# Kernel tuning notes

Hardware: AMD Instinct MI355X
Metric: run time of the kernel (lower is better)

Reference implementation:

```python
import jax, jax.numpy as jnp
import numpy as np

N = 8192
D = 128
NUM_CLASSES = 16
EPS = 1e-8  # torch cosine_similarity eps


def setup_inputs() -> dict:
    key = jax.random.key(0)
    k1, k2 = jax.random.split(key)
    inp = jax.random.normal(k1, (N, D), dtype=jnp.float32)
    targets = jax.random.randint(k2, (N,), 0, NUM_CLASSES, dtype=jnp.int64)
    temperature = jnp.asarray(0.5, dtype=jnp.float32)
    return {"input": inp, "targets": targets, "temperature": temperature}


def reference(input, targets, temperature):
    # clamp temperature to [0.1, 1.0] as the module does in forward
    temp = jnp.clip(temperature, 0.1, 1.0)

    # cosine similarity matrix [N, N]
    norms = jnp.maximum(jnp.linalg.norm(input, axis=1, keepdims=True), EPS)
    xn = input / norms
    sim = jnp.matmul(xn, xn.T) / temp          # [N, N]
    E = jnp.exp(sim)                            # [N, N]

    same = targets[:, None] == targets[None, :]  # [N, N] bool
    diag = jnp.diagonal(E)                       # exp(s_ii)
    pos = jnp.sum(jnp.where(same, E, 0.0), axis=1) - diag   # same-class, excl self
    tot = jnp.sum(E, axis=1) - diag                          # pos + neg
    per_sample_loss = -jnp.log(pos / tot)                    # [N]

    # per-class aggregation (segment sums with static num_segments)
    counts = jax.ops.segment_sum(jnp.ones_like(per_sample_loss), targets,
                                 num_segments=NUM_CLASSES)
    sums = jax.ops.segment_sum(per_sample_loss, targets,
                               num_segments=NUM_CLASSES)
    safe_counts = jnp.maximum(counts, 1.0)
    class_mean = sums / safe_counts

    # class weights: (1/count) normalized over present classes
    inv = jnp.where(counts > 0, 1.0 / safe_counts, 0.0)
    weights = inv / jnp.sum(inv)

    # only classes with more than one sample contribute
    valid = counts > 1
    weighted = jnp.where(valid, class_mean * weights, 0.0)
    n_valid = jnp.sum(valid.astype(jnp.float32))
    loss = jnp.sum(weighted) / n_valid
    return loss
```

## Files before the change

kernel.cpp:

```cpp
#include <hip/hip_runtime.h>

#define N 8192
#define D 128
#define NCLS 16
#define SLOT 512
#define RSTRIDE 256

typedef unsigned short u16;
typedef __attribute__((ext_vector_type(8))) short v8s;
typedef __attribute__((ext_vector_type(16))) float f32x16;

static __device__ inline u16 f2bf(float f) {
  unsigned int u = __builtin_bit_cast(unsigned int, f);
  unsigned int r = u + 0x7fffu + ((u >> 16) & 1u);
  return (u16)(r >> 16);
}

__global__ __launch_bounds__(256) void k_norm(float* __restrict__ buf,
                                              const float* __restrict__ temp) {
  int wave = threadIdx.x >> 6;
  int lane = threadIdx.x & 63;
  int row = blockIdx.x * 4 + wave;
  const float* p = buf + (size_t)row * D + lane * 2;
  float x = p[0], y = p[1];
  float ss = x * x + y * y;
#pragma unroll
  for (int m = 32; m >= 1; m >>= 1) ss += __shfl_xor(ss, m);
  float t = fminf(fmaxf(temp[0], 0.1f), 1.0f);
  float sc = sqrtf(1.4426950408889634f / t);
  float inv = sc / fmaxf(sqrtf(ss), 1e-8f);
  unsigned int u0 = (unsigned int)f2bf(x * inv);
  unsigned int u1 = (unsigned int)f2bf(y * inv);
  reinterpret_cast<unsigned int*>(buf)[(size_t)row * 128 + lane] = u0 | (u1 << 16);
}

__global__ __launch_bounds__(256, 3) void k_sim(float* __restrict__ buf,
                                                const int* __restrict__ tgt) {
  __shared__ __align__(16) char lds[2][64 * 256];
  __shared__ float red_pos[4][32];
  __shared__ float red_tot[4][32];

  const int tid = threadIdx.x;
  const int wave = tid >> 6;
  const int lane = tid & 63;
  const int l31 = lane & 31;
  const int h = lane >> 5;

  const u16* xnb = reinterpret_cast<const u16*>(buf);

  const int rowstrip = blockIdx.x >> 3;
  const int cq = blockIdx.x & 7;
  const int rwb = rowstrip * 64 + (wave >> 1) * 32;
  const int colblock = cq * 1024;
  const int ch = wave & 1;

  v8s afrag[8];
  {
    const u16* ap = xnb + (size_t)(rwb + l31) * RSTRIDE + h * 8;
#pragma unroll
    for (int kk = 0; kk < 8; ++kk)
      afrag[kk] = *reinterpret_cast<const v8s*>(ap + kk * 16);
  }

  int trow[16];
#pragma unroll
  for (int r = 0; r < 16; ++r)
    trow[r] = tgt[rwb + ((r & 3) + 8 * (r >> 2) + 4 * h)];

  float tot_acc[16], pos_acc[16];
#pragma unroll
  for (int r = 0; r < 16; ++r) { tot_acc[r] = 0.f; pos_acc[r] = 0.f; }

  auto stage = [&](int g, int bsel) {
    int rowbase = colblock + g * 64;
#pragma unroll
    for (int i = 0; i < 4; ++i) {
      int L = i * 256 + tid;
      int row = L >> 4;
      int s = (L & 15) ^ (row & 15);
      const char* src = reinterpret_cast<const char*>(buf) +
                        (size_t)(rowbase + row) * SLOT + s * 16;
      char* dst = &lds[bsel][(i * 256 + wave * 64) * 16];
      __builtin_amdgcn_global_load_lds(
          (const __attribute__((address_space(1))) void*)src,
          (__attribute__((address_space(3))) void*)dst, 16, 0, 0);
    }
  };

  stage(0, 0);
  __syncthreads();

  const int lr = ch * 32 + l31;
  const int lbase = lr * 256;
  const int lm = lr & 15;

  for (int g = 0; g < 16; ++g) {
    int cur = g & 1;
    if (g + 1 < 16) stage(g + 1, cur ^ 1);

    int c0 = colblock + g * 64 + ch * 32;
    int tcol = tgt[c0 + l31];

    f32x16 acc;
#pragma unroll
    for (int r = 0; r < 16; ++r) acc[r] = 0.f;
    const char* lb = lds[cur];
#pragma unroll
    for (int kk = 0; kk < 8; ++kk) {
      v8s bf = *reinterpret_cast<const v8s*>(lb + lbase + (((2 * kk + h) ^ lm) << 4));
      acc = __builtin_amdgcn_mfma_f32_32x32x16_bf16(afrag[kk], bf, acc, 0, 0, 0);
    }

    if (c0 != rwb) {
#pragma unroll
      for (int r = 0; r < 16; ++r) {
        float e = exp2f(acc[r]);
        tot_acc[r] += e;
        pos_acc[r] += (tcol == trow[r]) ? e : 0.f;
      }
    } else {
#pragma unroll
      for (int r = 0; r < 16; ++r) {
        float e = exp2f(acc[r]);
        if (l31 == ((r & 3) + 8 * (r >> 2) + 4 * h)) e = 0.f;
        tot_acc[r] += e;
        pos_acc[r] += (tcol == trow[r]) ? e : 0.f;
      }
    }
    __syncthreads();
  }

#pragma unroll
  for (int r = 0; r < 16; ++r) {
    float p = pos_acc[r], q = tot_acc[r];
#pragma unroll
    for (int m = 1; m <= 16; m <<= 1) {
      p += __shfl_xor(p, m);
      q += __shfl_xor(q, m);
    }
    if (l31 == 0) {
      int rl = (r & 3) + 8 * (r >> 2) + 4 * h;
      red_pos[wave][rl] = p;
      red_tot[wave][rl] = q;
    }
  }
  __syncthreads();
  if (tid < 64) {
    int gg = tid >> 5, rl = tid & 31;
    int row = rowstrip * 64 + gg * 32 + rl;
    float p = red_pos[2 * gg][rl] + red_pos[2 * gg + 1][rl];
    float q = red_tot[2 * gg][rl] + red_tot[2 * gg + 1][rl];
    float* slot = reinterpret_cast<float*>(reinterpret_cast<char*>(buf) + (size_t)row * SLOT + 256);
    slot[cq] = p;
    slot[8 + cq] = q;
  }
}

__global__ __launch_bounds__(1024) void k_tail(const float* __restrict__ buf,
                                               const int* __restrict__ tgt,
                                               float* __restrict__ out) {
  __shared__ float cs[NCLS], cc[NCLS];
  int tid = threadIdx.x;
  if (tid < NCLS) { cs[tid] = 0.f; cc[tid] = 0.f; }
  __syncthreads();
#pragma unroll
  for (int j = 0; j < 8; ++j) {
    int row = j * 1024 + tid;
    const float4* s4 = reinterpret_cast<const float4*>(
        reinterpret_cast<const char*>(buf) + (size_t)row * SLOT + 256);
    float4 a = s4[0], b = s4[1], c4 = s4[2], d4 = s4[3];
    float pos = a.x + a.y + a.z + a.w + b.x + b.y + b.z + b.w;
    float tot = c4.x + c4.y + c4.z + c4.w + d4.x + d4.y + d4.z + d4.w;
    float loss = logf(tot) - logf(pos);
    int c = tgt[row];
    atomicAdd(&cs[c], loss);
    atomicAdd(&cc[c], 1.0f);
  }
  __syncthreads();
  if (tid < 64) {
    int c = tid;
    float s = 0.f, n = 0.f;
    if (c < NCLS) { s = cs[c]; n = cc[c]; }
    float safe = fmaxf(n, 1.0f);
    float mean = s / safe;
    float inv = (n > 0.5f) ? 1.0f / safe : 0.f;
    float valid = (n > 1.5f) ? 1.f : 0.f;
    float w = (n > 1.5f) ? mean * inv : 0.f;
    float sinv = inv, sw = w, sv = valid;
#pragma unroll
    for (int m = 1; m <= 32; m <<= 1) {
      sinv += __shfl_xor(sinv, m);
      sw += __shfl_xor(sw, m);
      sv += __shfl_xor(sv, m);
    }
    if (c == 0) out[0] = sw / sinv / sv;
  }
}

extern "C" void kernel_launch(void* const* d_in, const int* in_sizes, int n_in,
                              void* d_out, int out_size, void* d_ws, size_t ws_size,
                              hipStream_t stream) {
  float* buf = (float*)d_in[0];
  const int* tgt = (const int*)d_in[1];
  const float* temp = (const float*)d_in[2];
  float* out = (float*)d_out;
  (void)d_ws; (void)ws_size;

  k_norm<<<N / 4, 256, 0, stream>>>(buf, temp);
  k_sim<<<1024, 256, 0, stream>>>(buf, tgt);
  k_tail<<<1, 1024, 0, stream>>>(buf, tgt, out);
}
```

Measured before the change: 131.3 us.

## Retile similarity kernel to 128x256 blocks and split tail reduction across blocks

Each k_sim block now covers 128 rows by 256 columns. All four waves share one 32-column B tile staged into LDS per step, where before each tile was shared by two waves. Each wave writes its row partials straight to global, which removes the shared-memory cross-wave reduction and one barrier, and the grid doubles to 2048 blocks. The single-block tail is replaced by 64 blocks that compute per-class partial sums, followed by a tiny final kernel. The trade-offs are more partial slots per row (32 instead of 8), more global writes, and one extra kernel launch.

New measurement: 112.6 us. -14.3%, faster.

```diff
diff --git a/kernel.cpp b/kernel.cpp
--- a/kernel.cpp
+++ b/kernel.cpp
@@ -34,25 +34,23 @@
   reinterpret_cast<unsigned int*>(buf)[(size_t)row * 128 + lane] = u0 | (u1 << 16);
 }
 
-__global__ __launch_bounds__(256, 3) void k_sim(float* __restrict__ buf,
-                                                const int* __restrict__ tgt) {
-  __shared__ __align__(16) char lds[2][64 * 256];
-  __shared__ float red_pos[4][32];
-  __shared__ float red_tot[4][32];
+__global__ __launch_bounds__(256) void k_sim(float* __restrict__ buf,
+                                             const int* __restrict__ tgt) {
+  __shared__ __align__(16) char lds[2][32 * 256];
 
   const int tid = threadIdx.x;
   const int wave = tid >> 6;
   const int lane = tid & 63;
   const int l31 = lane & 31;
   const int h = lane >> 5;
+  const int lm = l31 & 15;
 
   const u16* xnb = reinterpret_cast<const u16*>(buf);
 
-  const int rowstrip = blockIdx.x >> 3;
-  const int cq = blockIdx.x & 7;
-  const int rwb = rowstrip * 64 + (wave >> 1) * 32;
-  const int colblock = cq * 1024;
-  const int ch = wave & 1;
+  const int rowstrip = blockIdx.x >> 5;
+  const int cq = blockIdx.x & 31;
+  const int rwb = rowstrip * 128 + wave * 32;
+  const int colblock = cq * 256;
 
   v8s afrag[8];
   {
@@ -72,9 +70,9 @@
   for (int r = 0; r < 16; ++r) { tot_acc[r] = 0.f; pos_acc[r] = 0.f; }
 
   auto stage = [&](int g, int bsel) {
-    int rowbase = colblock + g * 64;
-#pragma unroll
-    for (int i = 0; i < 4; ++i) {
+    int rowbase = colblock + g * 32;
+#pragma unroll
+    for (int i = 0; i < 2; ++i) {
       int L = i * 256 + tid;
       int row = L >> 4;
       int s = (L & 15) ^ (row & 15);
@@ -90,15 +88,13 @@
   stage(0, 0);
   __syncthreads();
 
-  const int lr = ch * 32 + l31;
-  const int lbase = lr * 256;
-  const int lm = lr & 15;
-
-  for (int g = 0; g < 16; ++g) {
+  const int lbase = l31 * 256;
+
+  for (int g = 0; g < 8; ++g) {
     int cur = g & 1;
-    if (g + 1 < 16) stage(g + 1, cur ^ 1);
-
-    int c0 = colblock + g * 64 + ch * 32;
+    if (g + 1 < 8) stage(g + 1, cur ^ 1);
+
+    int c0 = colblock + g * 32;
     int tcol = tgt[c0 + l31];
 
     f32x16 acc;
@@ -139,42 +135,55 @@
       q += __shfl_xor(q, m);
     }
     if (l31 == 0) {
-      int rl = (r & 3) + 8 * (r >> 2) + 4 * h;
-      red_pos[wave][rl] = p;
-      red_tot[wave][rl] = q;
-    }
-  }
-  __syncthreads();
-  if (tid < 64) {
-    int gg = tid >> 5, rl = tid & 31;
-    int row = rowstrip * 64 + gg * 32 + rl;
-    float p = red_pos[2 * gg][rl] + red_pos[2 * gg + 1][rl];
-    float q = red_tot[2 * gg][rl] + red_tot[2 * gg + 1][rl];
-    float* slot = reinterpret_cast<float*>(reinterpret_cast<char*>(buf) + (size_t)row * SLOT + 256);
-    slot[cq] = p;
-    slot[8 + cq] = q;
-  }
-}
-
-__global__ __launch_bounds__(1024) void k_tail(const float* __restrict__ buf,
-                                               const int* __restrict__ tgt,
-                                               float* __restrict__ out) {
+      int row = rwb + ((r & 3) + 8 * (r >> 2) + 4 * h);
+      float* slot = reinterpret_cast<float*>(
+          reinterpret_cast<char*>(buf) + (size_t)row * SLOT + 256);
+      slot[cq] = p;
+      slot[32 + cq] = q;
+    }
+  }
+}
+
+__global__ __launch_bounds__(128) void k_tail_a(float* __restrict__ buf,
+                                                const int* __restrict__ tgt) {
   __shared__ float cs[NCLS], cc[NCLS];
   int tid = threadIdx.x;
   if (tid < NCLS) { cs[tid] = 0.f; cc[tid] = 0.f; }
   __syncthreads();
-#pragma unroll
-  for (int j = 0; j < 8; ++j) {
-    int row = j * 1024 + tid;
-    const float4* s4 = reinterpret_cast<const float4*>(
-        reinterpret_cast<const char*>(buf) + (size_t)row * SLOT + 256);
-    float4 a = s4[0], b = s4[1], c4 = s4[2], d4 = s4[3];
-    float pos = a.x + a.y + a.z + a.w + b.x + b.y + b.z + b.w;
-    float tot = c4.x + c4.y + c4.z + c4.w + d4.x + d4.y + d4.z + d4.w;
-    float loss = logf(tot) - logf(pos);
-    int c = tgt[row];
-    atomicAdd(&cs[c], loss);
-    atomicAdd(&cc[c], 1.0f);
+  int row = blockIdx.x * 128 + tid;
+  const float4* s4 = reinterpret_cast<const float4*>(
+      reinterpret_cast<const char*>(buf) + (size_t)row * SLOT + 256);
+  float pos = 0.f, tot = 0.f;
+#pragma unroll
+  for (int i = 0; i < 8; ++i) {
+    float4 a = s4[i], b = s4[8 + i];
+    pos += a.x + a.y + a.z + a.w;
+    tot += b.x + b.y + b.z + b.w;
+  }
+  float loss = logf(tot) - logf(pos);
+  int c = tgt[row];
+  atomicAdd(&cs[c], loss);
+  atomicAdd(&cc[c], 1.0f);
+  __syncthreads();
+  if (tid < 2 * NCLS) {
+    float* dst = reinterpret_cast<float*>(
+        reinterpret_cast<char*>(buf) + (size_t)blockIdx.x * SLOT);
+    dst[tid] = (tid < NCLS) ? cs[tid] : cc[tid - NCLS];
+  }
+}
+
+__global__ __launch_bounds__(1024) void k_final(const float* __restrict__ buf,
+                                                float* __restrict__ out) {
+  __shared__ float cs[NCLS], cc[NCLS];
+  int tid = threadIdx.x;
+  if (tid < NCLS) { cs[tid] = 0.f; cc[tid] = 0.f; }
+  __syncthreads();
+  {
+    int b = tid >> 4, c = tid & 15;
+    const float* src = reinterpret_cast<const float*>(
+        reinterpret_cast<const char*>(buf) + (size_t)b * SLOT);
+    atomicAdd(&cs[c], src[c]);
+    atomicAdd(&cc[c], src[NCLS + c]);
   }
   __syncthreads();
   if (tid < 64) {
@@ -207,6 +216,7 @@
   (void)d_ws; (void)ws_size;
 
   k_norm<<<N / 4, 256, 0, stream>>>(buf, temp);
-  k_sim<<<1024, 256, 0, stream>>>(buf, tgt);
-  k_tail<<<1, 1024, 0, stream>>>(buf, tgt, out);
-}
+  k_sim<<<2048, 256, 0, stream>>>(buf, tgt);
+  k_tail_a<<<64, 128, 0, stream>>>(buf, tgt);
+  k_final<<<1, 1024, 0, stream>>>(buf, out);
+}
```
